# Kernel optimization log

Hardware: AMD Instinct MI355X
Metric: run time of the kernel (lower is better)

The kernel has to match this reference:

```python
import jax, jax.numpy as jnp
import numpy as np

N_EMBD = 768
N_HEAD = 12
B, T = 2, 2048
EPS = 1e-5


def _layernorm(x, g, b):
    mu = jnp.mean(x, axis=-1, keepdims=True)
    var = jnp.var(x, axis=-1, keepdims=True)
    return (x - mu) * jax.lax.rsqrt(var + EPS) * g + b


def _mha(q, k, v, causal):
    # q,k,v: [B,T,C] already projected
    Bq, Tq, C = q.shape
    d = C // N_HEAD
    q = q.reshape(Bq, Tq, N_HEAD, d).transpose(0, 2, 1, 3)  # b h t d
    k = k.reshape(Bq, Tq, N_HEAD, d).transpose(0, 2, 1, 3)
    v = v.reshape(Bq, Tq, N_HEAD, d).transpose(0, 2, 1, 3)
    scores = jnp.einsum('bhqd,bhkd->bhqk', q, k) * (1.0 / jnp.sqrt(jnp.float32(d)))
    if causal:
        mask = jnp.tril(jnp.ones((Tq, Tq), dtype=bool))
        scores = jnp.where(mask[None, None], scores, jnp.float32(-jnp.inf))
    att = jax.nn.softmax(scores, axis=-1)
    y = jnp.einsum('bhqk,bhkd->bhqd', att, v)
    return y.transpose(0, 2, 1, 3).reshape(Bq, Tq, C)


def setup_inputs() -> dict:
    key = jax.random.key(0)
    ks = iter(jax.random.split(key, 32))
    C = N_EMBD

    def lin(kk, din, dout):
        w = jax.random.normal(kk, (din, dout), jnp.float32) * (1.0 / np.sqrt(din))
        return w

    inp = {
        'x': jax.random.normal(next(ks), (B, T, C), jnp.float32),
        'encoder_output': jax.random.normal(next(ks), (B, T, C), jnp.float32),
        'ln1_g': jnp.ones((C,), jnp.float32), 'ln1_b': jnp.zeros((C,), jnp.float32),
        'attn_qkv_w': lin(next(ks), C, 3 * C), 'attn_qkv_b': jnp.zeros((3 * C,), jnp.float32),
        'attn_proj_w': lin(next(ks), C, C), 'attn_proj_b': jnp.zeros((C,), jnp.float32),
        'ln2_g': jnp.ones((C,), jnp.float32), 'ln2_b': jnp.zeros((C,), jnp.float32),
        'ca_q_w': lin(next(ks), C, C), 'ca_q_b': jnp.zeros((C,), jnp.float32),
        'ca_k_w': lin(next(ks), C, C), 'ca_k_b': jnp.zeros((C,), jnp.float32),
        'ca_v_w': lin(next(ks), C, C), 'ca_v_b': jnp.zeros((C,), jnp.float32),
        'ca_o_w': lin(next(ks), C, C), 'ca_o_b': jnp.zeros((C,), jnp.float32),
        'ln3_g': jnp.ones((C,), jnp.float32), 'ln3_b': jnp.zeros((C,), jnp.float32),
        'fc_w': lin(next(ks), C, 4 * C), 'fc_b': jnp.zeros((4 * C,), jnp.float32),
        'fc2_w': lin(next(ks), 4 * C, C), 'fc2_b': jnp.zeros((C,), jnp.float32),
    }
    return inp


def reference(x, encoder_output, ln1_g, ln1_b, attn_qkv_w, attn_qkv_b,
              attn_proj_w, attn_proj_b, ln2_g, ln2_b,
              ca_q_w, ca_q_b, ca_k_w, ca_k_b, ca_v_w, ca_v_b, ca_o_w, ca_o_b,
              ln3_g, ln3_b, fc_w, fc_b, fc2_w, fc2_b):
    C = N_EMBD
    # causal self-attention
    qkv = x @ attn_qkv_w + attn_qkv_b
    q, k, v = qkv[..., :C], qkv[..., C:2 * C], qkv[..., 2 * C:]
    sa = _mha(q, k, v, causal=True) @ attn_proj_w + attn_proj_b
    x = _layernorm(sa + x, ln1_g, ln1_b)
    # cross-attention
    cq = x @ ca_q_w + ca_q_b
    ck = encoder_output @ ca_k_w + ca_k_b
    cv = encoder_output @ ca_v_w + ca_v_b
    ca = _mha(cq, ck, cv, causal=False) @ ca_o_w + ca_o_b
    x = _layernorm(ca + x, ln2_g, ln2_b)
    # MLP
    h = jax.nn.relu(x @ fc_w + fc_b) @ fc2_w + fc2_b
    x = _layernorm(h + x, ln3_g, ln3_b)
    return x
```

## Files before the change

kernel.cpp:

```cpp
#include <hip/hip_runtime.h>


#define C_EMBD 768
#define NHEAD  12
#define HD     64
#define TB     2048
#define BB     2
#define MTOK   (BB*TB)

typedef __bf16 bf16_8 __attribute__((ext_vector_type(8)));
typedef float  f32x4  __attribute__((ext_vector_type(4)));

#if __has_builtin(__builtin_amdgcn_exp2f)
#define EXP2(x) __builtin_amdgcn_exp2f(x)
#else
#define EXP2(x) exp2f(x)
#endif

__device__ __forceinline__ unsigned short f2bf(float f) {
    union { float f; unsigned u; } x; x.f = f;
    unsigned r = x.u + 0x7FFFu + ((x.u >> 16) & 1u);
    return (unsigned short)(r >> 16);
}

#define GLOAD_LDS16(gsrc, ldst) \
    __builtin_amdgcn_global_load_lds( \
        (const __attribute__((address_space(1))) void*)(gsrc), \
        (__attribute__((address_space(3))) void*)(ldst), 16, 0, 0)

__global__ __launch_bounds__(256) void k_conv_bf16(const float* __restrict__ in,
                                                   unsigned short* __restrict__ out) {
    int i = blockIdx.x * 256 + threadIdx.x;
    float4 v = ((const float4*)in)[i];
    ushort4 o;
    o.x = f2bf(v.x); o.y = f2bf(v.y); o.z = f2bf(v.z); o.w = f2bf(v.w);
    ((ushort4*)out)[i] = o;
}

__global__ __launch_bounds__(256) void k_concat_bias(const float* __restrict__ a,
                                                     const float* __restrict__ b,
                                                     float* __restrict__ dst) {
    int i = blockIdx.x * 256 + threadIdx.x;
    if (i < C_EMBD) { dst[i] = a[i]; dst[C_EMBD + i] = b[i]; }
}

__global__ __launch_bounds__(256) void k_transpose_w(const float* __restrict__ W,
                                                     unsigned short* __restrict__ Wt,
                                                     int K, int N) {
    __shared__ float tile[32][33];
    int tx = threadIdx.x, ty = threadIdx.y;
    int n0 = blockIdx.x * 32, k0 = blockIdx.y * 32;
#pragma unroll
    for (int i = 0; i < 4; ++i)
        tile[ty + 8*i][tx] = W[(size_t)(k0 + ty + 8*i) * N + n0 + tx];
    __syncthreads();
#pragma unroll
    for (int i = 0; i < 4; ++i)
        Wt[(size_t)(n0 + ty + 8*i) * K + k0 + tx] = f2bf(tile[tx][ty + 8*i]);
}

template<int BM, bool OUT_BF16, bool ADD_RES, bool RELU>
__global__ __launch_bounds__(256) void k_gemm_bt(
        const unsigned short* __restrict__ A,
        const unsigned short* __restrict__ Bt,
        const float* __restrict__ bias,
        const float* __restrict__ res,
        void* __restrict__ Cout,
        int M, int N, int K) {
    constexpr int MF = BM / 32;
    __shared__ unsigned short As[BM * 32];
    __shared__ unsigned short Bs[128 * 32];
    int tid  = threadIdx.x;
    int lane = tid & 63, wave = tid >> 6;
    int l16 = lane & 15, lg = lane >> 4;
    int wm = (wave >> 1) * (BM / 2), wn = (wave & 1) * 64;
    int bm = blockIdx.x * BM, bn = blockIdx.y * 128;

    f32x4 acc[MF][4] = {};

    for (int k0 = 0; k0 < K; k0 += 32) {
        __syncthreads();
#pragma unroll
        for (int i = 0; i < BM / 64; ++i) {
            int chunk = i * 256 + tid;
            GLOAD_LDS16(A + (size_t)(bm + (chunk >> 2)) * K + k0 + (chunk & 3) * 8,
                        As + (size_t)(i * 256 + wave * 64) * 8);
        }
#pragma unroll
        for (int i = 0; i < 2; ++i) {
            int chunk = i * 256 + tid;
            GLOAD_LDS16(Bt + (size_t)(bn + (chunk >> 2)) * K + k0 + (chunk & 3) * 8,
                        Bs + (size_t)(i * 256 + wave * 64) * 8);
        }
        __syncthreads();
        bf16_8 af[MF], bfr[4];
#pragma unroll
        for (int m = 0; m < MF; ++m)
            af[m]  = *(const bf16_8*)(As + (size_t)(wm + m*16 + l16) * 32 + lg * 8);
#pragma unroll
        for (int n = 0; n < 4; ++n)
            bfr[n] = *(const bf16_8*)(Bs + (size_t)(wn + n*16 + l16) * 32 + lg * 8);
#pragma unroll
        for (int m = 0; m < MF; ++m)
#pragma unroll
            for (int n = 0; n < 4; ++n)
                acc[m][n] = __builtin_amdgcn_mfma_f32_16x16x32_bf16(af[m], bfr[n], acc[m][n], 0, 0, 0);
    }

#pragma unroll
    for (int m = 0; m < MF; ++m) {
#pragma unroll
        for (int n = 0; n < 4; ++n) {
            int col = bn + wn + n*16 + l16;
            float bv = bias[col];
#pragma unroll
            for (int r = 0; r < 4; ++r) {
                int row = bm + wm + m*16 + lg*4 + r;
                float v = acc[m][n][r] + bv;
                if (ADD_RES) v += res[(size_t)row * N + col];
                if (RELU)    v = fmaxf(v, 0.f);
                if (OUT_BF16) ((unsigned short*)Cout)[(size_t)row * N + col] = f2bf(v);
                else          ((float*)Cout)[(size_t)row * N + col] = v;
            }
        }
    }
}

template<bool CAUSAL>
__global__ __launch_bounds__(256) void k_attn(
        const unsigned short* __restrict__ Qp,
        const unsigned short* __restrict__ Kp,
        const unsigned short* __restrict__ Vp,
        unsigned short* __restrict__ Yp,
        int strideQ, int strideKV, float scale2 ) {
    __shared__ unsigned short Ks[64][72];
    __shared__ unsigned short Vt[64][72];
    __shared__ unsigned short Ps[4][16][72];
    int tid  = threadIdx.x;
    int lane = tid & 63, wave = tid >> 6;
    int l16 = lane & 15, lg = lane >> 4;
    int bh = blockIdx.y;
    int b = bh / NHEAD, h = bh - b * NHEAD;
    int qt = CAUSAL ? (gridDim.x - 1 - blockIdx.x) : blockIdx.x;
    int wq = qt * 64 + wave * 16;

    const unsigned short* Qb = Qp + (size_t)b * TB * strideQ  + h * HD;
    const unsigned short* Kb = Kp + (size_t)b * TB * strideKV + h * HD;
    const unsigned short* Vb = Vp + (size_t)b * TB * strideKV + h * HD;

    bf16_8 qf0 = *(const bf16_8*)(Qb + (size_t)(wq + l16) * strideQ + lg * 8);
    bf16_8 qf1 = *(const bf16_8*)(Qb + (size_t)(wq + l16) * strideQ + 32 + lg * 8);

    bf16_8 vones;
#pragma unroll
    for (int j = 0; j < 8; ++j) vones[j] = (__bf16)1.0f;

    int vk2 = (tid & 31) * 2;
    int vd0 = (tid >> 5) * 8;

    f32x4 o[4] = {};
    float m_run[4], l_run[4];
#pragma unroll
    for (int r = 0; r < 4; ++r) { m_run[r] = -1e30f; l_run[r] = 0.f; }

    int ktEnd = CAUSAL ? (qt + 1) : (TB / 64);
    for (int kt = 0; kt < ktEnd; ++kt) {
        __syncthreads();
#pragma unroll
        for (int i = 0; i < 2; ++i) {
            int chunk = tid + i * 256;
            int r = chunk >> 3, cc = (chunk & 7) * 8;
            *(int4*)(&Ks[r][cc]) = *(const int4*)(Kb + (size_t)(kt*64 + r) * strideKV + cc);
        }
        {
            int4 va = *(const int4*)(Vb + (size_t)(kt*64 + vk2)     * strideKV + vd0);
            int4 vb = *(const int4*)(Vb + (size_t)(kt*64 + vk2 + 1) * strideKV + vd0);
            const unsigned short* pa = (const unsigned short*)&va;
            const unsigned short* pb = (const unsigned short*)&vb;
#pragma unroll
            for (int j = 0; j < 8; ++j) {
                unsigned pack = (unsigned)pa[j] | ((unsigned)pb[j] << 16);
                *(unsigned*)(&Vt[vd0 + j][vk2]) = pack;
            }
        }
        __syncthreads();

        f32x4 s[4];
#pragma unroll
        for (int n = 0; n < 4; ++n) {
            f32x4 z = {};
            bf16_8 kf0 = *(const bf16_8*)(&Ks[n*16 + l16][lg*8]);
            bf16_8 kf1 = *(const bf16_8*)(&Ks[n*16 + l16][32 + lg*8]);
            z = __builtin_amdgcn_mfma_f32_16x16x32_bf16(qf0, kf0, z, 0, 0, 0);
            z = __builtin_amdgcn_mfma_f32_16x16x32_bf16(qf1, kf1, z, 0, 0, 0);
            s[n] = z;
        }
#pragma unroll
        for (int n = 0; n < 4; ++n)
#pragma unroll
            for (int r = 0; r < 4; ++r) {
                float v = s[n][r] * scale2;
                if (CAUSAL) {
                    int kpos = kt*64 + n*16 + l16;
                    int qpos = wq + lg*4 + r;
                    if (kpos > qpos) v = -1e30f;
                }
                s[n][r] = v;
            }
        float mx[4];
#pragma unroll
        for (int r = 0; r < 4; ++r)
            mx[r] = fmaxf(fmaxf(s[0][r], s[1][r]), fmaxf(s[2][r], s[3][r]));
#pragma unroll
        for (int off = 1; off < 16; off <<= 1)
#pragma unroll
            for (int r = 0; r < 4; ++r)
                mx[r] = fmaxf(mx[r], __shfl_xor(mx[r], off, 64));
        float sf[4];
#pragma unroll
        for (int r = 0; r < 4; ++r) {
            float mnew = fmaxf(m_run[r], mx[r]);
            sf[r] = EXP2(m_run[r] - mnew);
            m_run[r] = mnew;
        }
#pragma unroll
        for (int n = 0; n < 4; ++n)
#pragma unroll
            for (int r = 0; r < 4; ++r)
                s[n][r] = EXP2(s[n][r] - m_run[r]);
#pragma unroll
        for (int n = 0; n < 4; ++n)
#pragma unroll
            for (int r = 0; r < 4; ++r) o[n][r] *= sf[r];

#pragma unroll
        for (int n = 0; n < 4; ++n)
#pragma unroll
            for (int r = 0; r < 4; ++r)
                Ps[wave][lg*4 + r][n*16 + l16] = f2bf(s[n][r]);
        __syncthreads();

        f32x4 zsum = {};
#pragma unroll
        for (int kk = 0; kk < 2; ++kk) {
            bf16_8 pa = *(const bf16_8*)(&Ps[wave][l16][kk*32 + lg*8]);
            zsum = __builtin_amdgcn_mfma_f32_16x16x32_bf16(pa, vones, zsum, 0, 0, 0);
#pragma unroll
            for (int n = 0; n < 4; ++n) {
                bf16_8 vf = *(const bf16_8*)(&Vt[n*16 + l16][kk*32 + lg*8]);
                o[n] = __builtin_amdgcn_mfma_f32_16x16x32_bf16(pa, vf, o[n], 0, 0, 0);
            }
        }
#pragma unroll
        for (int r = 0; r < 4; ++r) l_run[r] = l_run[r] * sf[r] + zsum[r];
    }

#pragma unroll
    for (int n = 0; n < 4; ++n)
#pragma unroll
        for (int r = 0; r < 4; ++r) {
            int token = b * TB + wq + lg*4 + r;
            float val = o[n][r] / l_run[r];
            Yp[(size_t)token * C_EMBD + h * HD + n*16 + l16] = f2bf(val);
        }
}

template<bool WF32, bool WBF16>
__global__ __launch_bounds__(256) void k_ln(const float* __restrict__ in,
                                            const float* __restrict__ g,
                                            const float* __restrict__ bb,
                                            float* __restrict__ outf,
                                            unsigned short* __restrict__ outb) {
    int row = blockIdx.x;
    const float* x = in + (size_t)row * C_EMBD;
    float v[3], s1 = 0.f, s2 = 0.f;
#pragma unroll
    for (int i = 0; i < 3; ++i) {
        v[i] = x[threadIdx.x + i * 256];
        s1 += v[i];
        s2 += v[i] * v[i];
    }
#pragma unroll
    for (int off = 1; off < 64; off <<= 1) {
        s1 += __shfl_xor(s1, off, 64);
        s2 += __shfl_xor(s2, off, 64);
    }
    __shared__ float red[8];
    int wave = threadIdx.x >> 6, lane = threadIdx.x & 63;
    if (lane == 0) { red[wave] = s1; red[4 + wave] = s2; }
    __syncthreads();
    s1 = red[0] + red[1] + red[2] + red[3];
    s2 = red[4] + red[5] + red[6] + red[7];
    float mu  = s1 * (1.f / C_EMBD);
    float var = s2 * (1.f / C_EMBD) - mu * mu;
    float rs  = rsqrtf(var + 1e-5f);
#pragma unroll
    for (int i = 0; i < 3; ++i) {
        int c = threadIdx.x + i * 256;
        float y = (v[i] - mu) * rs * g[c] + bb[c];
        if (WF32)  outf[(size_t)row * C_EMBD + c] = y;
        if (WBF16) outb[(size_t)row * C_EMBD + c] = f2bf(y);
    }
}

extern "C" void kernel_launch(void* const* d_in, const int* in_sizes, int n_in,
                              void* d_out, int out_size, void* d_ws, size_t ws_size,
                              hipStream_t stream) {
    (void)in_sizes; (void)n_in; (void)out_size; (void)ws_size;
    const float* x      = (const float*)d_in[0];
    const float* enc    = (const float*)d_in[1];
    const float* ln1_g  = (const float*)d_in[2];
    const float* ln1_b  = (const float*)d_in[3];
    const float* qkv_w  = (const float*)d_in[4];
    const float* qkv_b  = (const float*)d_in[5];
    const float* proj_w = (const float*)d_in[6];
    const float* proj_b = (const float*)d_in[7];
    const float* ln2_g  = (const float*)d_in[8];
    const float* ln2_b  = (const float*)d_in[9];
    const float* caq_w  = (const float*)d_in[10];
    const float* caq_b  = (const float*)d_in[11];
    const float* cak_w  = (const float*)d_in[12];
    const float* cak_b  = (const float*)d_in[13];
    const float* cav_w  = (const float*)d_in[14];
    const float* cav_b  = (const float*)d_in[15];
    const float* cao_w  = (const float*)d_in[16];
    const float* cao_b  = (const float*)d_in[17];
    const float* ln3_g  = (const float*)d_in[18];
    const float* ln3_b  = (const float*)d_in[19];
    const float* fc_w   = (const float*)d_in[20];
    const float* fc_b   = (const float*)d_in[21];
    const float* fc2_w  = (const float*)d_in[22];
    const float* fc2_b  = (const float*)d_in[23];
    float* out = (float*)d_out;

    char* ws = (char*)d_ws;
    auto us = [&](size_t off) { return (unsigned short*)(ws + off); };
    auto fl = [&](size_t off) { return (float*)(ws + off); };

    const size_t O_WQKV  = 0;
    const size_t O_WPROJ = 3538944;
    const size_t O_WCQ   = 4718592;
    const size_t O_WCK   = 5898240;
    const size_t O_WCV   = 7077888;
    const size_t O_WCO   = 8257536;
    const size_t O_WFC   = 9437184;
    const size_t O_WFC2  = 14155776;
    const size_t O_XBF   = 18874368;
    const size_t O_ENCBF = 25165824;
    const size_t O_QKVBF = 31457280;
    const size_t O_Q2    = O_QKVBF;
    const size_t O_KV2   = O_QKVBF + 6291456;
    const size_t O_YBF   = 50331648;
    const size_t O_RESF  = 56623104;
    const size_t O_X1F   = 69206016;
    const size_t O_X1BF  = 81788928;
    const size_t O_X2F   = 88080384;
    const size_t O_X2BF  = 100663296;
    const size_t O_HBF   = 106954752;
    const size_t O_BKV   = O_HBF;

    const float SC2 = 0.125f * 1.44269504f;
    dim3 tb(32, 8);

    k_conv_bf16<<<3072, 256, 0, stream>>>(x,   us(O_XBF));
    k_conv_bf16<<<3072, 256, 0, stream>>>(enc, us(O_ENCBF));
    k_concat_bias<<<3, 256, 0, stream>>>(cak_b, cav_b, fl(O_BKV));

    k_transpose_w<<<dim3(2304/32,  768/32), tb, 0, stream>>>(qkv_w,  us(O_WQKV),  768, 2304);
    k_transpose_w<<<dim3( 768/32,  768/32), tb, 0, stream>>>(proj_w, us(O_WPROJ), 768,  768);
    k_transpose_w<<<dim3( 768/32,  768/32), tb, 0, stream>>>(caq_w,  us(O_WCQ),   768,  768);
    k_transpose_w<<<dim3( 768/32,  768/32), tb, 0, stream>>>(cak_w,  us(O_WCK),   768,  768);
    k_transpose_w<<<dim3( 768/32,  768/32), tb, 0, stream>>>(cav_w,  us(O_WCV),   768,  768);
    k_transpose_w<<<dim3( 768/32,  768/32), tb, 0, stream>>>(cao_w,  us(O_WCO),   768,  768);
    k_transpose_w<<<dim3(3072/32,  768/32), tb, 0, stream>>>(fc_w,   us(O_WFC),   768, 3072);
    k_transpose_w<<<dim3( 768/32, 3072/32), tb, 0, stream>>>(fc2_w,  us(O_WFC2), 3072,  768);

    k_gemm_bt<128, true,  false, false><<<dim3(32, 18), 256, 0, stream>>>(
        us(O_XBF), us(O_WQKV), qkv_b, nullptr, us(O_QKVBF), MTOK, 2304, 768);
    k_attn<true><<<dim3(TB/64, BB*NHEAD), 256, 0, stream>>>(
        us(O_QKVBF), us(O_QKVBF) + 768, us(O_QKVBF) + 1536, us(O_YBF), 2304, 2304, SC2);
    k_gemm_bt<64, false, true,  false><<<dim3(64, 6), 256, 0, stream>>>(
        us(O_YBF), us(O_WPROJ), proj_b, x, fl(O_RESF), MTOK, 768, 768);
    k_ln<true, true><<<MTOK, 256, 0, stream>>>(fl(O_RESF), ln1_g, ln1_b, fl(O_X1F), us(O_X1BF));
    k_gemm_bt<64, true,  false, false><<<dim3(64, 6), 256, 0, stream>>>(
        us(O_X1BF),  us(O_WCQ), caq_b, nullptr, us(O_Q2), MTOK, 768, 768);
    k_gemm_bt<128, true,  false, false><<<dim3(32, 12), 256, 0, stream>>>(
        us(O_ENCBF), us(O_WCK), fl(O_BKV), nullptr, us(O_KV2), MTOK, 1536, 768);
    k_attn<false><<<dim3(TB/64, BB*NHEAD), 256, 0, stream>>>(
        us(O_Q2), us(O_KV2), us(O_KV2) + 768, us(O_YBF), 768, 1536, SC2);
    k_gemm_bt<64, false, true,  false><<<dim3(64, 6), 256, 0, stream>>>(
        us(O_YBF), us(O_WCO), cao_b, fl(O_X1F), fl(O_RESF), MTOK, 768, 768);
    k_ln<true, true><<<MTOK, 256, 0, stream>>>(fl(O_RESF), ln2_g, ln2_b, fl(O_X2F), us(O_X2BF));
    k_gemm_bt<128, true,  false, true ><<<dim3(32, 24), 256, 0, stream>>>(
        us(O_X2BF), us(O_WFC), fc_b, nullptr, us(O_HBF), MTOK, 3072, 768);
    k_gemm_bt<64, false, true,  false><<<dim3(64, 6), 256, 0, stream>>>(
        us(O_HBF), us(O_WFC2), fc2_b, fl(O_X2F), fl(O_RESF), MTOK, 768, 3072);
    k_ln<true, false><<<MTOK, 256, 0, stream>>>(fl(O_RESF), ln3_g, ln3_b, out, nullptr);
}
```

Baseline: 540.2 us.

## Prefetch K/V into registers, fold softmax scale into Q weights, lazy rescale

The attention kernel now loads the next K/V tile into registers while the current tile is being computed, so global latency overlaps with MFMA work. The softmax scale is folded into the Q projection weights and biases, so the attention kernel no longer multiplies every score. The causal mask is applied only on the diagonal tile. Running-max rescaling of the output and sum is skipped unless the max grows by more than 8 (log2 units), and the barrier before the per-wave P·V step is removed. Together these cut VALU work and synchronisation in the attention inner loop, at the cost of more register pressure and slightly different rounding from the unnormalised exponentials.

```diff
diff --git a/kernel.cpp b/kernel.cpp
--- a/kernel.cpp
+++ b/kernel.cpp
@@ -11,16 +11,12 @@
 typedef __bf16 bf16_8 __attribute__((ext_vector_type(8)));
 typedef float  f32x4  __attribute__((ext_vector_type(4)));
 
-#if __has_builtin(__builtin_amdgcn_exp2f)
-#define EXP2(x) __builtin_amdgcn_exp2f(x)
-#else
 #define EXP2(x) exp2f(x)
-#endif
 
 __device__ __forceinline__ unsigned short f2bf(float f) {
-    union { float f; unsigned u; } x; x.f = f;
-    unsigned r = x.u + 0x7FFFu + ((x.u >> 16) & 1u);
-    return (unsigned short)(r >> 16);
+    union { __bf16 h; unsigned short u; } c;
+    c.h = (__bf16)f;
+    return c.u;
 }
 
 #define GLOAD_LDS16(gsrc, ldst) \
@@ -44,9 +40,17 @@
     if (i < C_EMBD) { dst[i] = a[i]; dst[C_EMBD + i] = b[i]; }
 }
 
+__global__ __launch_bounds__(256) void k_scale_bias(const float* __restrict__ b,
+                                                    float* __restrict__ dst,
+                                                    int n, float s, int lim) {
+    int i = blockIdx.x * 256 + threadIdx.x;
+    if (i < n) dst[i] = b[i] * (i < lim ? s : 1.0f);
+}
+
 __global__ __launch_bounds__(256) void k_transpose_w(const float* __restrict__ W,
                                                      unsigned short* __restrict__ Wt,
-                                                     int K, int N) {
+                                                     int K, int N,
+                                                     float scale, int scaleLim) {
     __shared__ float tile[32][33];
     int tx = threadIdx.x, ty = threadIdx.y;
     int n0 = blockIdx.x * 32, k0 = blockIdx.y * 32;
@@ -55,8 +59,11 @@
         tile[ty + 8*i][tx] = W[(size_t)(k0 + ty + 8*i) * N + n0 + tx];
     __syncthreads();
 #pragma unroll
-    for (int i = 0; i < 4; ++i)
-        Wt[(size_t)(n0 + ty + 8*i) * K + k0 + tx] = f2bf(tile[tx][ty + 8*i]);
+    for (int i = 0; i < 4; ++i) {
+        int nrow = n0 + ty + 8*i;
+        float s = (nrow < scaleLim) ? scale : 1.0f;
+        Wt[(size_t)nrow * K + k0 + tx] = f2bf(tile[tx][ty + 8*i] * s);
+    }
 }
 
 template<int BM, bool OUT_BF16, bool ADD_RES, bool RELU>
@@ -132,10 +139,10 @@
         const unsigned short* __restrict__ Kp,
         const unsigned short* __restrict__ Vp,
         unsigned short* __restrict__ Yp,
-        int strideQ, int strideKV, float scale2 ) {
-    __shared__ unsigned short Ks[64][72];
-    __shared__ unsigned short Vt[64][72];
-    __shared__ unsigned short Ps[4][16][72];
+        int strideQ, int strideKV) {
+    __shared__ __bf16 Ks[64][72];
+    __shared__ __bf16 Vt[64][72];
+    __shared__ __bf16 Ps[4][16][72];
     int tid  = threadIdx.x;
     int lane = tid & 63, wave = tid >> 6;
     int l16 = lane & 15, lg = lane >> 4;
@@ -155,8 +162,26 @@
 #pragma unroll
     for (int j = 0; j < 8; ++j) vones[j] = (__bf16)1.0f;
 
+    int kr = tid >> 3, kc = (tid & 7) * 8;
     int vk2 = (tid & 31) * 2;
     int vd0 = (tid >> 5) * 8;
+
+    const unsigned short* gK0 = Kb + (size_t)kr  * strideKV + kc;
+    const unsigned short* gK1 = gK0 + (size_t)32 * strideKV;
+    const unsigned short* gV0 = Vb + (size_t)vk2 * strideKV + vd0;
+    const unsigned short* gV1 = gV0 + strideKV;
+    const size_t stepKV = (size_t)64 * strideKV;
+
+    int4 kA = *(const int4*)gK0;
+    int4 kB = *(const int4*)gK1;
+    unsigned vp[8];
+    {
+        int4 va = *(const int4*)gV0, vb2 = *(const int4*)gV1;
+        const unsigned short* pa = (const unsigned short*)&va;
+        const unsigned short* pb = (const unsigned short*)&vb2;
+#pragma unroll
+        for (int j = 0; j < 8; ++j) vp[j] = (unsigned)pa[j] | ((unsigned)pb[j] << 16);
+    }
 
     f32x4 o[4] = {};
     float m_run[4], l_run[4];
@@ -166,24 +191,23 @@
     int ktEnd = CAUSAL ? (qt + 1) : (TB / 64);
     for (int kt = 0; kt < ktEnd; ++kt) {
         __syncthreads();
-#pragma unroll
-        for (int i = 0; i < 2; ++i) {
-            int chunk = tid + i * 256;
-            int r = chunk >> 3, cc = (chunk & 7) * 8;
-            *(int4*)(&Ks[r][cc]) = *(const int4*)(Kb + (size_t)(kt*64 + r) * strideKV + cc);
-        }
-        {
-            int4 va = *(const int4*)(Vb + (size_t)(kt*64 + vk2)     * strideKV + vd0);
-            int4 vb = *(const int4*)(Vb + (size_t)(kt*64 + vk2 + 1) * strideKV + vd0);
+        *(int4*)(&Ks[kr][kc])      = kA;
+        *(int4*)(&Ks[kr + 32][kc]) = kB;
+#pragma unroll
+        for (int j = 0; j < 8; ++j)
+            *(unsigned*)(&Vt[vd0 + j][vk2]) = vp[j];
+        __syncthreads();
+
+        if (kt + 1 < ktEnd) {
+            gK0 += stepKV; gK1 += stepKV; gV0 += stepKV; gV1 += stepKV;
+            kA = *(const int4*)gK0;
+            kB = *(const int4*)gK1;
+            int4 va = *(const int4*)gV0, vb2 = *(const int4*)gV1;
             const unsigned short* pa = (const unsigned short*)&va;
-            const unsigned short* pb = (const unsigned short*)&vb;
-#pragma unroll
-            for (int j = 0; j < 8; ++j) {
-                unsigned pack = (unsigned)pa[j] | ((unsigned)pb[j] << 16);
-                *(unsigned*)(&Vt[vd0 + j][vk2]) = pack;
-            }
-        }
-        __syncthreads();
+            const unsigned short* pb = (const unsigned short*)&vb2;
+#pragma unroll
+            for (int j = 0; j < 8; ++j) vp[j] = (unsigned)pa[j] | ((unsigned)pb[j] << 16);
+        }
 
         f32x4 s[4];
 #pragma unroll
@@ -195,18 +219,13 @@
             z = __builtin_amdgcn_mfma_f32_16x16x32_bf16(qf1, kf1, z, 0, 0, 0);
             s[n] = z;
         }
-#pragma unroll
-        for (int n = 0; n < 4; ++n)
-#pragma unroll
-            for (int r = 0; r < 4; ++r) {
-                float v = s[n][r] * scale2;
-                if (CAUSAL) {
-                    int kpos = kt*64 + n*16 + l16;
-                    int qpos = wq + lg*4 + r;
-                    if (kpos > qpos) v = -1e30f;
-                }
-                s[n][r] = v;
-            }
+        if (CAUSAL && kt == qt) {
+#pragma unroll
+            for (int n = 0; n < 4; ++n)
+#pragma unroll
+                for (int r = 0; r < 4; ++r)
+                    if (kt*64 + n*16 + l16 > wq + lg*4 + r) s[n][r] = -1e30f;
+        }
         float mx[4];
 #pragma unroll
         for (int r = 0; r < 4; ++r)
@@ -216,29 +235,24 @@
 #pragma unroll
             for (int r = 0; r < 4; ++r)
                 mx[r] = fmaxf(mx[r], __shfl_xor(mx[r], off, 64));
-        float sf[4];
-#pragma unroll
-        for (int r = 0; r < 4; ++r) {
-            float mnew = fmaxf(m_run[r], mx[r]);
-            sf[r] = EXP2(m_run[r] - mnew);
-            m_run[r] = mnew;
+        bool big = (mx[0] > m_run[0] + 8.f) | (mx[1] > m_run[1] + 8.f) |
+                   (mx[2] > m_run[2] + 8.f) | (mx[3] > m_run[3] + 8.f);
+        if (__any(big)) {
+#pragma unroll
+            for (int r = 0; r < 4; ++r) {
+                float mnew = fmaxf(m_run[r], mx[r]);
+                float sf = EXP2(m_run[r] - mnew);
+                m_run[r] = mnew;
+                l_run[r] *= sf;
+#pragma unroll
+                for (int n = 0; n < 4; ++n) o[n][r] *= sf;
+            }
         }
 #pragma unroll
         for (int n = 0; n < 4; ++n)
 #pragma unroll
             for (int r = 0; r < 4; ++r)
-                s[n][r] = EXP2(s[n][r] - m_run[r]);
-#pragma unroll
-        for (int n = 0; n < 4; ++n)
-#pragma unroll
-            for (int r = 0; r < 4; ++r) o[n][r] *= sf[r];
-
-#pragma unroll
-        for (int n = 0; n < 4; ++n)
-#pragma unroll
-            for (int r = 0; r < 4; ++r)
-                Ps[wave][lg*4 + r][n*16 + l16] = f2bf(s[n][r]);
-        __syncthreads();
+                Ps[wave][lg*4 + r][n*16 + l16] = (__bf16)EXP2(s[n][r] - m_run[r]);
 
         f32x4 zsum = {};
 #pragma unroll
@@ -252,17 +266,17 @@
             }
         }
 #pragma unroll
-        for (int r = 0; r < 4; ++r) l_run[r] = l_run[r] * sf[r] + zsum[r];
-    }
-
-#pragma unroll
-    for (int n = 0; n < 4; ++n)
-#pragma unroll
-        for (int r = 0; r < 4; ++r) {
-            int token = b * TB + wq + lg*4 + r;
-            float val = o[n][r] / l_run[r];
-            Yp[(size_t)token * C_EMBD + h * HD + n*16 + l16] = f2bf(val);
-        }
+        for (int r = 0; r < 4; ++r) l_run[r] += zsum[r];
+    }
+
+#pragma unroll
+    for (int r = 0; r < 4; ++r) {
+        float rl = 1.0f / l_run[r];
+        int token = b * TB + wq + lg*4 + r;
+#pragma unroll
+        for (int n = 0; n < 4; ++n)
+            Yp[(size_t)token * C_EMBD + h * HD + n*16 + l16] = f2bf(o[n][r] * rl);
+    }
 }
 
 template<bool WF32, bool WBF16>
@@ -358,6 +372,8 @@
     const size_t O_X2BF  = 100663296;
     const size_t O_HBF   = 106954752;
     const size_t O_BKV   = O_HBF;
+    const size_t O_BQKV  = O_HBF + 8192;
+    const size_t O_BCQ   = O_HBF + 20480;
 
     const float SC2 = 0.125f * 1.44269504f;
     dim3 tb(32, 8);
@@ -365,29 +381,31 @@
     k_conv_bf16<<<3072, 256, 0, stream>>>(x,   us(O_XBF));
     k_conv_bf16<<<3072, 256, 0, stream>>>(enc, us(O_ENCBF));
     k_concat_bias<<<3, 256, 0, stream>>>(cak_b, cav_b, fl(O_BKV));
-
-    k_transpose_w<<<dim3(2304/32,  768/32), tb, 0, stream>>>(qkv_w,  us(O_WQKV),  768, 2304);
-    k_transpose_w<<<dim3( 768/32,  768/32), tb, 0, stream>>>(proj_w, us(O_WPROJ), 768,  768);
-    k_transpose_w<<<dim3( 768/32,  768/32), tb, 0, stream>>>(caq_w,  us(O_WCQ),   768,  768);
-    k_transpose_w<<<dim3( 768/32,  768/32), tb, 0, stream>>>(cak_w,  us(O_WCK),   768,  768);
-    k_transpose_w<<<dim3( 768/32,  768/32), tb, 0, stream>>>(cav_w,  us(O_WCV),   768,  768);
-    k_transpose_w<<<dim3( 768/32,  768/32), tb, 0, stream>>>(cao_w,  us(O_WCO),   768,  768);
-    k_transpose_w<<<dim3(3072/32,  768/32), tb, 0, stream>>>(fc_w,   us(O_WFC),   768, 3072);
-    k_transpose_w<<<dim3( 768/32, 3072/32), tb, 0, stream>>>(fc2_w,  us(O_WFC2), 3072,  768);
+    k_scale_bias<<<9, 256, 0, stream>>>(qkv_b, fl(O_BQKV), 2304, SC2, 768);
+    k_scale_bias<<<3, 256, 0, stream>>>(caq_b, fl(O_BCQ),   768, SC2, 768);
+
+    k_transpose_w<<<dim3(2304/32,  768/32), tb, 0, stream>>>(qkv_w,  us(O_WQKV),  768, 2304, SC2, 768);
+    k_transpose_w<<<dim3( 768/32,  768/32), tb, 0, stream>>>(proj_w, us(O_WPROJ), 768,  768, 1.f, 0);
+    k_transpose_w<<<dim3( 768/32,  768/32), tb, 0, stream>>>(caq_w,  us(O_WCQ),   768,  768, SC2, 768);
+    k_transpose_w<<<dim3( 768/32,  768/32), tb, 0, stream>>>(cak_w,  us(O_WCK),   768,  768, 1.f, 0);
+    k_transpose_w<<<dim3( 768/32,  768/32), tb, 0, stream>>>(cav_w,  us(O_WCV),   768,  768, 1.f, 0);
+    k_transpose_w<<<dim3( 768/32,  768/32), tb, 0, stream>>>(cao_w,  us(O_WCO),   768,  768, 1.f, 0);
+    k_transpose_w<<<dim3(3072/32,  768/32), tb, 0, stream>>>(fc_w,   us(O_WFC),   768, 3072, 1.f, 0);
+    k_transpose_w<<<dim3( 768/32, 3072/32), tb, 0, stream>>>(fc2_w,  us(O_WFC2), 3072,  768, 1.f, 0);
 
     k_gemm_bt<128, true,  false, false><<<dim3(32, 18), 256, 0, stream>>>(
-        us(O_XBF), us(O_WQKV), qkv_b, nullptr, us(O_QKVBF), MTOK, 2304, 768);
+        us(O_XBF), us(O_WQKV), fl(O_BQKV), nullptr, us(O_QKVBF), MTOK, 2304, 768);
     k_attn<true><<<dim3(TB/64, BB*NHEAD), 256, 0, stream>>>(
-        us(O_QKVBF), us(O_QKVBF) + 768, us(O_QKVBF) + 1536, us(O_YBF), 2304, 2304, SC2);
+        us(O_QKVBF), us(O_QKVBF) + 768, us(O_QKVBF) + 1536, us(O_YBF), 2304, 2304);
     k_gemm_bt<64, false, true,  false><<<dim3(64, 6), 256, 0, stream>>>(
         us(O_YBF), us(O_WPROJ), proj_b, x, fl(O_RESF), MTOK, 768, 768);
     k_ln<true, true><<<MTOK, 256, 0, stream>>>(fl(O_RESF), ln1_g, ln1_b, fl(O_X1F), us(O_X1BF));
     k_gemm_bt<64, true,  false, false><<<dim3(64, 6), 256, 0, stream>>>(
-        us(O_X1BF),  us(O_WCQ), caq_b, nullptr, us(O_Q2), MTOK, 768, 768);
+        us(O_X1BF),  us(O_WCQ), fl(O_BCQ), nullptr, us(O_Q2), MTOK, 768, 768);
     k_gemm_bt<128, true,  false, false><<<dim3(32, 12), 256, 0, stream>>>(
         us(O_ENCBF), us(O_WCK), fl(O_BKV), nullptr, us(O_KV2), MTOK, 1536, 768);
     k_attn<false><<<dim3(TB/64, BB*NHEAD), 256, 0, stream>>>(
-        us(O_Q2), us(O_KV2), us(O_KV2) + 768, us(O_YBF), 768, 1536, SC2);
+        us(O_Q2), us(O_KV2), us(O_KV2) + 768, us(O_YBF), 768, 1536);
     k_gemm_bt<64, false, true,  false><<<dim3(64, 6), 256, 0, stream>>>(
         us(O_YBF), us(O_WCO), cao_b, fl(O_X1F), fl(O_RESF), MTOK, 768, 768);
     k_ln<true, true><<<MTOK, 256, 0, stream>>>(fl(O_RESF), ln2_g, ln2_b, fl(O_X2F), us(O_X2BF));
```

Measured after the change: 531.2 us. No clear change (-1.7%).
